# Performance work log

Hardware: AMD Instinct MI355X
Metric: run time of the kernel (lower is better)

## Reference

```python
import jax, jax.numpy as jnp
import numpy as np

NUM_CLASSES = 4   # Level has 4 contiguous classes 0..3
VMAX = 64         # discretized vital-sign codes live in [0, VMAX)
HID = 64
OUT = 768
IN_VS = 28


def casual_weighted(vs, labels):
    """Vectorized equivalent of Encoder.CasualWeighted.

    For row i, col c: prob = (# rows j with labels[j]==labels[i] and
    vs[j,c]==vs[i,c]) / (# rows with labels==labels[i]).  Returns vs * prob.
    """
    N, F = vs.shape
    vs_int = vs.astype(jnp.int32)                       # values are integer codes
    lab = labels.astype(jnp.int32)
    keys = lab[:, None] * VMAX + vs_int                 # [N, F] joint (class, value) key
    cols = jnp.arange(F)[None, :]                       # [1, F]
    counts = jnp.zeros((NUM_CLASSES * VMAX, F), jnp.float32).at[keys, cols].add(1.0)
    class_size = jnp.zeros((NUM_CLASSES,), jnp.float32).at[lab].add(1.0)
    prob = counts[keys, cols] / class_size[lab][:, None]  # [N, F]
    return vs * prob


def feature_extractor(x, W_ih, W_hh, b_ih, b_hh, W_fc, b_fc):
    """nn.LSTM over a length-1 sequence (h0=c0=0) followed by Linear."""
    h0 = jnp.zeros((x.shape[0], HID), x.dtype)
    gates = x @ W_ih.T + h0 @ W_hh.T + b_ih + b_hh      # [N, 4H], torch gate order i,f,g,o
    i, f, g, o = jnp.split(gates, 4, axis=-1)
    c = jax.nn.sigmoid(i) * jnp.tanh(g)                 # f*c0 = 0
    h = jax.nn.sigmoid(o) * jnp.tanh(c)
    return h @ W_fc.T + b_fc                            # [N, OUT]


def setup_inputs() -> dict:
    key = jax.random.key(0)
    ks = jax.random.split(key, 10)
    N = 100000
    VS = jax.random.randint(ks[0], (N, IN_VS), 0, VMAX).astype(jnp.float32)
    CC = jax.random.normal(ks[1], (N, 1, OUT), dtype=jnp.float32)
    Level = jax.random.randint(ks[2], (N,), 0, NUM_CLASSES).astype(jnp.int64)
    Depart = jax.random.randint(ks[3], (N,), 0, 10).astype(jnp.int64)
    s = 0.05
    W_ih = jax.random.normal(ks[4], (4 * HID, IN_VS), dtype=jnp.float32) * s
    W_hh = jax.random.normal(ks[5], (4 * HID, HID), dtype=jnp.float32) * s
    b_ih = jax.random.normal(ks[6], (4 * HID,), dtype=jnp.float32) * s
    b_hh = jax.random.normal(ks[7], (4 * HID,), dtype=jnp.float32) * s
    W_fc = jax.random.normal(ks[8], (OUT, HID), dtype=jnp.float32) * s
    b_fc = jax.random.normal(ks[9], (OUT,), dtype=jnp.float32) * s
    return {"VS": VS, "CC": CC, "Level": Level, "Depart": Depart,
            "W_ih": W_ih, "W_hh": W_hh, "b_ih": b_ih, "b_hh": b_hh,
            "W_fc": W_fc, "b_fc": b_fc}


def reference(VS, CC, Level, Depart, W_ih, W_hh, b_ih, b_hh, W_fc, b_fc):
    cc_feat = jnp.squeeze(CC)                           # [N, 768]
    vs_cw = casual_weighted(VS, Level)                  # [N, 28]
    vs_feat = feature_extractor(vs_cw, W_ih, W_hh, b_ih, b_hh, W_fc, b_fc)
    return (cc_feat, vs_feat, Level, Depart)
```

## Files before the change

### kernel.cpp

```cpp
#include <hip/hip_runtime.h>
#include <hip/hip_bf16.h>

#define N_ROWS 100000
#define F_VS 28
#define HIDN 64
#define OUT_F 768
#define NCLS 4
#define VMAXC 64

#define TILE_BLOCKS 1563
#define COPY_BLOCKS 485
#define GRID_FUSED (TILE_BLOCKS + COPY_BLOCKS)

typedef __attribute__((ext_vector_type(8))) short short8;
typedef __attribute__((ext_vector_type(4))) float floatx4;


__device__ __forceinline__ float frcp(float x) { return __builtin_amdgcn_rcpf(x); }
__device__ __forceinline__ float sigm(float x) { return frcp(1.f + __expf(-x)); }
__device__ __forceinline__ float tanh_f(float x) { return 1.f - 2.f * frcp(__expf(2.f * x) + 1.f); }

__global__ __launch_bounds__(256) void k_hist(const float* __restrict__ VS,
                                              const int* __restrict__ Level,
                                              const float* __restrict__ Wfc,
                                              int* __restrict__ counts,
                                              int* __restrict__ cls,
                                              __hip_bfloat16* __restrict__ wfc16) {
    __shared__ int lc[NCLS * VMAXC * F_VS];
    __shared__ int lcls[NCLS];
    int tid = threadIdx.x;
    for (int i = tid; i < NCLS * VMAXC * F_VS; i += 256) lc[i] = 0;
    if (tid < NCLS) lcls[tid] = 0;

    int gtid = blockIdx.x * 256 + tid;
    int gsz = gridDim.x * 256;
    for (int i = gtid; i < OUT_F * HIDN; i += gsz)
        wfc16[i] = __float2bfloat16(Wfc[i]);
    __syncthreads();

    for (int i = gtid; i < N_ROWS; i += gsz) {
        int lab = Level[i];
        atomicAdd(&lcls[lab], 1);
        const float4* row = (const float4*)(VS + (size_t)i * F_VS);
#pragma unroll
        for (int q = 0; q < 7; q++) {
            float4 v4 = row[q];
            int c = q * 4;
            atomicAdd(&lc[((lab << 6) + (int)v4.x) * F_VS + c + 0], 1);
            atomicAdd(&lc[((lab << 6) + (int)v4.y) * F_VS + c + 1], 1);
            atomicAdd(&lc[((lab << 6) + (int)v4.z) * F_VS + c + 2], 1);
            atomicAdd(&lc[((lab << 6) + (int)v4.w) * F_VS + c + 3], 1);
        }
    }
    __syncthreads();
    for (int i = tid; i < NCLS * VMAXC * F_VS; i += 256) {
        int v = lc[i];
        if (v) atomicAdd(&counts[i], v);
    }
    if (tid < NCLS) {
        int v = lcls[tid];
        if (v) atomicAdd(&cls[tid], v);
    }
}

__global__ __launch_bounds__(256) void k_fused(const float* __restrict__ VS,
                                               const int* __restrict__ Level,
                                               const int* __restrict__ Depart,
                                               const float* __restrict__ Wih,
                                               const float* __restrict__ bih,
                                               const float* __restrict__ bhh,
                                               const int* __restrict__ counts,
                                               const int* __restrict__ cls,
                                               const __hip_bfloat16* __restrict__ wfc16,
                                               const float* __restrict__ bfc,
                                               const float4* __restrict__ CC,
                                               float4* __restrict__ outCC,
                                               float* __restrict__ outV,
                                               float* __restrict__ outL,
                                               float* __restrict__ outD) {
    int tid = threadIdx.x;

    if (blockIdx.x >= TILE_BLOCKS) {
        int cb = blockIdx.x - TILE_BLOCKS;
        int ctid = cb * 256 + tid;
        int csz = COPY_BLOCKS * 256;
        for (int i = ctid; i < N_ROWS; i += csz) {
            outL[i] = (float)Level[i];
            outD[i] = (float)Depart[i];
        }
        const int n4 = (N_ROWS * OUT_F) / 4;
        for (int i = ctid; i < n4; i += csz) outCC[i] = CC[i];
        return;
    }

    int lane = tid & 63;
    int wib = tid >> 6;
    int wave = blockIdx.x * 4 + wib;
    const int nm = N_ROWS / 16;
    if (wave >= nm) return;

    float w0[F_VS], w2[F_VS], w3[F_VS];
#pragma unroll
    for (int j = 0; j < F_VS; j++) {
        w0[j] = Wih[(0 * HIDN + lane) * F_VS + j];
        w2[j] = Wih[(2 * HIDN + lane) * F_VS + j];
        w3[j] = Wih[(3 * HIDN + lane) * F_VS + j];
    }
    float b0 = bih[0 * HIDN + lane] + bhh[0 * HIDN + lane];
    float b2 = bih[2 * HIDN + lane] + bhh[2 * HIDN + lane];
    float b3 = bih[3 * HIDN + lane] + bhh[3 * HIDN + lane];

    __shared__ float xsh[4][64];
    __shared__ short hsh[4][16][72];

    int row0 = wave * 16;
#pragma unroll 1
    for (int i = 0; i < 16; i++) {
        int r = row0 + i;
        int lab = Level[r];
        float inv = frcp((float)cls[lab]);
        float xv = 0.f;
        if (lane < F_VS) {
            float v = VS[(size_t)r * F_VS + lane];
            int vi = (int)v;
            int cnt = counts[(((lab << 6) | vi)) * F_VS + lane];
            xv = v * ((float)cnt * inv);
        }
        xsh[wib][lane] = xv;
        __asm__ volatile("" ::: "memory");

        float a0 = b0, a2 = b2, a3 = b3;
#pragma unroll
        for (int q = 0; q < 7; q++) {
            floatx4 xq = *(const floatx4*)(&xsh[wib][q * 4]);
            a0 = fmaf(xq[0], w0[4 * q + 0], a0);
            a0 = fmaf(xq[1], w0[4 * q + 1], a0);
            a0 = fmaf(xq[2], w0[4 * q + 2], a0);
            a0 = fmaf(xq[3], w0[4 * q + 3], a0);
            a2 = fmaf(xq[0], w2[4 * q + 0], a2);
            a2 = fmaf(xq[1], w2[4 * q + 1], a2);
            a2 = fmaf(xq[2], w2[4 * q + 2], a2);
            a2 = fmaf(xq[3], w2[4 * q + 3], a2);
            a3 = fmaf(xq[0], w3[4 * q + 0], a3);
            a3 = fmaf(xq[1], w3[4 * q + 1], a3);
            a3 = fmaf(xq[2], w3[4 * q + 2], a3);
            a3 = fmaf(xq[3], w3[4 * q + 3], a3);
        }
        __asm__ volatile("" ::: "memory");

        float c = sigm(a0) * tanh_f(a2);
        float h = sigm(a3) * tanh_f(c);
        __hip_bfloat16 hb = __float2bfloat16(h);
        hsh[wib][i][lane] = *(short*)&hb;
    }
    __asm__ volatile("" ::: "memory");

    int quad = lane >> 4;
    int l16 = lane & 15;
    const short* hA = &hsh[wib][l16][quad * 8];
    short8 a0v = *(const short8*)(hA);
    short8 a1v = *(const short8*)(hA + 32);

    for (int nt = 0; nt < OUT_F / 16; nt++) {
        const short* pB = (const short*)(wfc16 + (size_t)(nt * 16 + l16) * HIDN + quad * 8);
        short8 bf0 = *(const short8*)(pB);
        short8 bf1 = *(const short8*)(pB + 32);
        floatx4 acc = {0.f, 0.f, 0.f, 0.f};
        acc = __builtin_amdgcn_mfma_f32_16x16x32_bf16(a0v, bf0, acc, 0, 0, 0);
        acc = __builtin_amdgcn_mfma_f32_16x16x32_bf16(a1v, bf1, acc, 0, 0, 0);
        float bias = bfc[nt * 16 + l16];
#pragma unroll
        for (int rr = 0; rr < 4; rr++) {
            outV[(size_t)(row0 + quad * 4 + rr) * OUT_F + nt * 16 + l16] = acc[rr] + bias;
        }
    }
}

extern "C" void kernel_launch(void* const* d_in, const int* in_sizes, int n_in,
                              void* d_out, int out_size, void* d_ws, size_t ws_size,
                              hipStream_t stream) {
    const float* VS = (const float*)d_in[0];
    const float* CC = (const float*)d_in[1];
    const int* Level = (const int*)d_in[2];
    const int* Depart = (const int*)d_in[3];
    const float* Wih = (const float*)d_in[4];
    const float* bih = (const float*)d_in[6];
    const float* bhh = (const float*)d_in[7];
    const float* Wfc = (const float*)d_in[8];
    const float* bfc = (const float*)d_in[9];

    float* out = (float*)d_out;
    char* ws = (char*)d_ws;
    int* counts = (int*)ws;
    int* cls = (int*)(ws + 28672);
    __hip_bfloat16* wfc16 = (__hip_bfloat16*)(ws + 28928);

    float* outCC = out;
    float* outV = out + (size_t)N_ROWS * OUT_F;
    float* outL = out + (size_t)2 * N_ROWS * OUT_F;
    float* outD = outL + N_ROWS;

    hipMemsetAsync(d_ws, 0, 28688, stream);
    k_hist<<<64, 256, 0, stream>>>(VS, Level, Wfc, counts, cls, wfc16);
    k_fused<<<GRID_FUSED, 256, 0, stream>>>(VS, Level, Depart, Wih, bih, bhh,
                                            counts, cls, wfc16, bfc,
                                            (const float4*)CC, (float4*)outCC,
                                            outV, outL, outD);
}
```

Baseline: 890.9 us.

## Split CC copy between histogram kernel and atomic work-stealing chunks in fused kernel

The histogram launch grows to 256 blocks, and the extra 192 blocks copy the first part of the CC passthrough while the histogram runs. The rest of the copy becomes atomic-counter work stealing in chunks: both the copy blocks and the LSTM/MFMA tile waves pull chunks once their own work is done. The aim is to balance the memory-bound copy across all blocks and overlap it with the histogram phase, replacing a fixed static split. In exchange it adds an atomic per chunk and uses one more workspace counter that must be zeroed by the memset.

```diff
diff --git a/kernel.cpp b/kernel.cpp
--- a/kernel.cpp
+++ b/kernel.cpp
@@ -12,6 +12,10 @@
 #define COPY_BLOCKS 485
 #define GRID_FUSED (TILE_BLOCKS + COPY_BLOCKS)
 
+#define N4_TOTAL (N_ROWS * OUT_F / 4)
+#define COPY_A   1572864
+#define CHUNKW   16384
+
 typedef __attribute__((ext_vector_type(8))) short short8;
 typedef __attribute__((ext_vector_type(4))) float floatx4;
 
@@ -19,25 +23,56 @@
 __device__ __forceinline__ float frcp(float x) { return __builtin_amdgcn_rcpf(x); }
 __device__ __forceinline__ float sigm(float x) { return frcp(1.f + __expf(-x)); }
 __device__ __forceinline__ float tanh_f(float x) { return 1.f - 2.f * frcp(__expf(2.f * x) + 1.f); }
+
+__device__ __forceinline__ void steal_copy(const float4* __restrict__ CC,
+                                           float4* __restrict__ outCC,
+                                           int* __restrict__ ctr, int lane) {
+    const int nchunks = (N4_TOTAL - COPY_A + CHUNKW - 1) / CHUNKW;
+    for (;;) {
+        int c = 0;
+        if (lane == 0) c = atomicAdd(ctr, 1);
+        c = __shfl(c, 0);
+        if (c >= nchunks) break;
+        int base = COPY_A + c * CHUNKW;
+        int end = base + CHUNKW;
+        if (end > N4_TOTAL) end = N4_TOTAL;
+        for (int i = base + lane; i < end; i += 64) outCC[i] = CC[i];
+    }
+}
 
 __global__ __launch_bounds__(256) void k_hist(const float* __restrict__ VS,
                                               const int* __restrict__ Level,
                                               const float* __restrict__ Wfc,
                                               int* __restrict__ counts,
                                               int* __restrict__ cls,
-                                              __hip_bfloat16* __restrict__ wfc16) {
+                                              __hip_bfloat16* __restrict__ wfc16,
+                                              const float4* __restrict__ CC,
+                                              float4* __restrict__ outCC) {
+    int tid = threadIdx.x;
+    int b = blockIdx.x;
+
+    {
+        int gtid = b * 256 + tid;
+        int gsz = 256 * 256;
+        for (int i = gtid; i < OUT_F * HIDN; i += gsz)
+            wfc16[i] = __float2bfloat16(Wfc[i]);
+    }
+
+    if (b >= 64) {
+        int ctid = (b - 64) * 256 + tid;
+        int csz = 192 * 256;
+        for (int i = ctid; i < COPY_A; i += csz) outCC[i] = CC[i];
+        return;
+    }
+
     __shared__ int lc[NCLS * VMAXC * F_VS];
     __shared__ int lcls[NCLS];
-    int tid = threadIdx.x;
     for (int i = tid; i < NCLS * VMAXC * F_VS; i += 256) lc[i] = 0;
     if (tid < NCLS) lcls[tid] = 0;
-
-    int gtid = blockIdx.x * 256 + tid;
-    int gsz = gridDim.x * 256;
-    for (int i = gtid; i < OUT_F * HIDN; i += gsz)
-        wfc16[i] = __float2bfloat16(Wfc[i]);
     __syncthreads();
 
+    int gtid = b * 256 + tid;
+    int gsz = 64 * 256;
     for (int i = gtid; i < N_ROWS; i += gsz) {
         int lab = Level[i];
         atomicAdd(&lcls[lab], 1);
@@ -77,8 +112,10 @@
                                                float4* __restrict__ outCC,
                                                float* __restrict__ outV,
                                                float* __restrict__ outL,
-                                               float* __restrict__ outD) {
+                                               float* __restrict__ outD,
+                                               int* __restrict__ ctr) {
     int tid = threadIdx.x;
+    int lane = tid & 63;
 
     if (blockIdx.x >= TILE_BLOCKS) {
         int cb = blockIdx.x - TILE_BLOCKS;
@@ -88,92 +125,93 @@
             outL[i] = (float)Level[i];
             outD[i] = (float)Depart[i];
         }
-        const int n4 = (N_ROWS * OUT_F) / 4;
-        for (int i = ctid; i < n4; i += csz) outCC[i] = CC[i];
+        steal_copy(CC, outCC, ctr, lane);
         return;
     }
 
-    int lane = tid & 63;
     int wib = tid >> 6;
     int wave = blockIdx.x * 4 + wib;
     const int nm = N_ROWS / 16;
-    if (wave >= nm) return;
-
-    float w0[F_VS], w2[F_VS], w3[F_VS];
-#pragma unroll
-    for (int j = 0; j < F_VS; j++) {
-        w0[j] = Wih[(0 * HIDN + lane) * F_VS + j];
-        w2[j] = Wih[(2 * HIDN + lane) * F_VS + j];
-        w3[j] = Wih[(3 * HIDN + lane) * F_VS + j];
-    }
-    float b0 = bih[0 * HIDN + lane] + bhh[0 * HIDN + lane];
-    float b2 = bih[2 * HIDN + lane] + bhh[2 * HIDN + lane];
-    float b3 = bih[3 * HIDN + lane] + bhh[3 * HIDN + lane];
 
     __shared__ float xsh[4][64];
     __shared__ short hsh[4][16][72];
 
-    int row0 = wave * 16;
+    if (wave < nm) {
+        float w0[F_VS], w2[F_VS], w3[F_VS];
+#pragma unroll
+        for (int j = 0; j < F_VS; j++) {
+            w0[j] = Wih[(0 * HIDN + lane) * F_VS + j];
+            w2[j] = Wih[(2 * HIDN + lane) * F_VS + j];
+            w3[j] = Wih[(3 * HIDN + lane) * F_VS + j];
+        }
+        float b0 = bih[0 * HIDN + lane] + bhh[0 * HIDN + lane];
+        float b2 = bih[2 * HIDN + lane] + bhh[2 * HIDN + lane];
+        float b3 = bih[3 * HIDN + lane] + bhh[3 * HIDN + lane];
+
+        int row0 = wave * 16;
 #pragma unroll 1
-    for (int i = 0; i < 16; i++) {
-        int r = row0 + i;
-        int lab = Level[r];
-        float inv = frcp((float)cls[lab]);
-        float xv = 0.f;
-        if (lane < F_VS) {
-            float v = VS[(size_t)r * F_VS + lane];
-            int vi = (int)v;
-            int cnt = counts[(((lab << 6) | vi)) * F_VS + lane];
-            xv = v * ((float)cnt * inv);
-        }
-        xsh[wib][lane] = xv;
+        for (int i = 0; i < 16; i++) {
+            int r = row0 + i;
+            int lab = Level[r];
+            float inv = frcp((float)cls[lab]);
+            float xv = 0.f;
+            if (lane < F_VS) {
+                float v = VS[(size_t)r * F_VS + lane];
+                int vi = (int)v;
+                int cnt = counts[(((lab << 6) | vi)) * F_VS + lane];
+                xv = v * ((float)cnt * inv);
+            }
+            xsh[wib][lane] = xv;
+            __asm__ volatile("" ::: "memory");
+
+            float a0 = b0, a2 = b2, a3 = b3;
+#pragma unroll
+            for (int q = 0; q < 7; q++) {
+                floatx4 xq = *(const floatx4*)(&xsh[wib][q * 4]);
+                a0 = fmaf(xq[0], w0[4 * q + 0], a0);
+                a0 = fmaf(xq[1], w0[4 * q + 1], a0);
+                a0 = fmaf(xq[2], w0[4 * q + 2], a0);
+                a0 = fmaf(xq[3], w0[4 * q + 3], a0);
+                a2 = fmaf(xq[0], w2[4 * q + 0], a2);
+                a2 = fmaf(xq[1], w2[4 * q + 1], a2);
+                a2 = fmaf(xq[2], w2[4 * q + 2], a2);
+                a2 = fmaf(xq[3], w2[4 * q + 3], a2);
+                a3 = fmaf(xq[0], w3[4 * q + 0], a3);
+                a3 = fmaf(xq[1], w3[4 * q + 1], a3);
+                a3 = fmaf(xq[2], w3[4 * q + 2], a3);
+                a3 = fmaf(xq[3], w3[4 * q + 3], a3);
+            }
+            __asm__ volatile("" ::: "memory");
+
+            float c = sigm(a0) * tanh_f(a2);
+            float h = sigm(a3) * tanh_f(c);
+            __hip_bfloat16 hb = __float2bfloat16(h);
+            hsh[wib][i][lane] = *(short*)&hb;
+        }
         __asm__ volatile("" ::: "memory");
 
-        float a0 = b0, a2 = b2, a3 = b3;
-#pragma unroll
-        for (int q = 0; q < 7; q++) {
-            floatx4 xq = *(const floatx4*)(&xsh[wib][q * 4]);
-            a0 = fmaf(xq[0], w0[4 * q + 0], a0);
-            a0 = fmaf(xq[1], w0[4 * q + 1], a0);
-            a0 = fmaf(xq[2], w0[4 * q + 2], a0);
-            a0 = fmaf(xq[3], w0[4 * q + 3], a0);
-            a2 = fmaf(xq[0], w2[4 * q + 0], a2);
-            a2 = fmaf(xq[1], w2[4 * q + 1], a2);
-            a2 = fmaf(xq[2], w2[4 * q + 2], a2);
-            a2 = fmaf(xq[3], w2[4 * q + 3], a2);
-            a3 = fmaf(xq[0], w3[4 * q + 0], a3);
-            a3 = fmaf(xq[1], w3[4 * q + 1], a3);
-            a3 = fmaf(xq[2], w3[4 * q + 2], a3);
-            a3 = fmaf(xq[3], w3[4 * q + 3], a3);
-        }
-        __asm__ volatile("" ::: "memory");
-
-        float c = sigm(a0) * tanh_f(a2);
-        float h = sigm(a3) * tanh_f(c);
-        __hip_bfloat16 hb = __float2bfloat16(h);
-        hsh[wib][i][lane] = *(short*)&hb;
-    }
-    __asm__ volatile("" ::: "memory");
-
-    int quad = lane >> 4;
-    int l16 = lane & 15;
-    const short* hA = &hsh[wib][l16][quad * 8];
-    short8 a0v = *(const short8*)(hA);
-    short8 a1v = *(const short8*)(hA + 32);
-
-    for (int nt = 0; nt < OUT_F / 16; nt++) {
-        const short* pB = (const short*)(wfc16 + (size_t)(nt * 16 + l16) * HIDN + quad * 8);
-        short8 bf0 = *(const short8*)(pB);
-        short8 bf1 = *(const short8*)(pB + 32);
-        floatx4 acc = {0.f, 0.f, 0.f, 0.f};
-        acc = __builtin_amdgcn_mfma_f32_16x16x32_bf16(a0v, bf0, acc, 0, 0, 0);
-        acc = __builtin_amdgcn_mfma_f32_16x16x32_bf16(a1v, bf1, acc, 0, 0, 0);
-        float bias = bfc[nt * 16 + l16];
-#pragma unroll
-        for (int rr = 0; rr < 4; rr++) {
-            outV[(size_t)(row0 + quad * 4 + rr) * OUT_F + nt * 16 + l16] = acc[rr] + bias;
-        }
-    }
+        int quad = lane >> 4;
+        int l16 = lane & 15;
+        const short* hA = &hsh[wib][l16][quad * 8];
+        short8 a0v = *(const short8*)(hA);
+        short8 a1v = *(const short8*)(hA + 32);
+
+        for (int nt = 0; nt < OUT_F / 16; nt++) {
+            const short* pB = (const short*)(wfc16 + (size_t)(nt * 16 + l16) * HIDN + quad * 8);
+            short8 bf0 = *(const short8*)(pB);
+            short8 bf1 = *(const short8*)(pB + 32);
+            floatx4 acc = {0.f, 0.f, 0.f, 0.f};
+            acc = __builtin_amdgcn_mfma_f32_16x16x32_bf16(a0v, bf0, acc, 0, 0, 0);
+            acc = __builtin_amdgcn_mfma_f32_16x16x32_bf16(a1v, bf1, acc, 0, 0, 0);
+            float bias = bfc[nt * 16 + l16];
+#pragma unroll
+            for (int rr = 0; rr < 4; rr++) {
+                outV[(size_t)(row0 + quad * 4 + rr) * OUT_F + nt * 16 + l16] = acc[rr] + bias;
+            }
+        }
+    }
+
+    steal_copy(CC, outCC, ctr, lane);
 }
 
 extern "C" void kernel_launch(void* const* d_in, const int* in_sizes, int n_in,
@@ -193,6 +231,7 @@
     char* ws = (char*)d_ws;
     int* counts = (int*)ws;
     int* cls = (int*)(ws + 28672);
+    int* ctr = (int*)(ws + 28688);
     __hip_bfloat16* wfc16 = (__hip_bfloat16*)(ws + 28928);
 
     float* outCC = out;
@@ -200,10 +239,11 @@
     float* outL = out + (size_t)2 * N_ROWS * OUT_F;
     float* outD = outL + N_ROWS;
 
-    hipMemsetAsync(d_ws, 0, 28688, stream);
-    k_hist<<<64, 256, 0, stream>>>(VS, Level, Wfc, counts, cls, wfc16);
+    hipMemsetAsync(d_ws, 0, 28692, stream);
+    k_hist<<<256, 256, 0, stream>>>(VS, Level, Wfc, counts, cls, wfc16,
+                                    (const float4*)CC, (float4*)outCC);
     k_fused<<<GRID_FUSED, 256, 0, stream>>>(VS, Level, Depart, Wih, bih, bhh,
                                             counts, cls, wfc16, bfc,
                                             (const float4*)CC, (float4*)outCC,
-                                            outV, outL, outD);
-}
+                                            outV, outL, outD, ctr);
+}
```

Result: slower. 1.099 ms (+23.3%).
